# Kernel optimization log

Hardware: AMD Instinct MI355X
Metric: run time of the kernel (lower is better)

## Reference

```python
import jax, jax.numpy as jnp
import numpy as np

H_DIM = 64
GRID = 8
NS = 2.0  # neighborhood_size
S = 256   # number of sequences (scenes)
P = 64    # pedestrians per sequence
EPS = 1e-5


def setup_inputs() -> dict:
    key = jax.random.key(0)
    k = jax.random.split(key, 6)
    N = S * P
    G = GRID * GRID
    h_states = jax.random.normal(k[0], (1, N, H_DIM), jnp.float32)
    end_pos = jax.random.normal(k[1], (N, 2), jnp.float32)
    starts = (jnp.arange(S, dtype=jnp.int32) * P)
    seq_start_end = jnp.stack([starts, starts + P], axis=1)  # (S, 2)
    # mlp_pool: Linear(G*H_DIM -> H_DIM) + BatchNorm1d + ReLU
    W = jax.random.normal(k[2], (G * H_DIM, H_DIM), jnp.float32) / np.sqrt(G * H_DIM)
    b = jnp.zeros((H_DIM,), jnp.float32)
    gamma = jnp.ones((H_DIM,), jnp.float32)
    beta = jnp.zeros((H_DIM,), jnp.float32)
    return {"h_states": h_states, "seq_start_end": seq_start_end, "end_pos": end_pos,
            "W": W, "b": b, "gamma": gamma, "beta": beta}


def reference(h_states, seq_start_end, end_pos, W, b, gamma, beta):
    nseq = seq_start_end.shape[0]          # S (static)
    N = end_pos.shape[0]
    Hd = h_states.shape[-1]
    nped = N // nseq                       # P (static; equal-length sequences)
    G = GRID * GRID
    half = NS / 2.0

    h = h_states.reshape(N, Hd).reshape(nseq, nped, Hd)     # (S, P, H)
    pos = end_pos.reshape(nseq, nped, 2)                    # (S, P, 2)

    # bounds per center pedestrian i
    tl_x = pos[..., 0] - half   # (S, P)
    tl_y = pos[..., 1] + half
    br_x = pos[..., 0] + half
    br_y = pos[..., 1] - half

    # pairwise: axis 1 = center i, axis 2 = other k
    ox = pos[:, None, :, 0]     # (S, 1, P)
    oy = pos[:, None, :, 1]
    cell_x = jnp.floor((ox - tl_x[:, :, None]) / NS * GRID)
    cell_y = jnp.floor((tl_y[:, :, None] - oy) / NS * GRID)
    grid = cell_x + cell_y * GRID                            # (S, P, P)

    oob = ((ox >= br_x[:, :, None]) | (ox <= tl_x[:, :, None]) |
           (oy >= tl_y[:, :, None]) | (oy <= br_y[:, :, None]))
    diag = jnp.eye(nped, dtype=bool)[None]                   # self excluded (within_bound[0::P+1]=1)
    valid = (~oob) & (~diag)

    grid_i = jnp.clip(grid.astype(jnp.int32), 0, G - 1)      # masked entries don't matter
    seq_off = (jnp.arange(nseq, dtype=jnp.int32)[:, None, None] * nped
               + jnp.arange(nped, dtype=jnp.int32)[None, :, None]) * G
    dummy = nseq * nped * G
    ids = jnp.where(valid, seq_off + grid_i, dummy)          # (S, P, P)

    # data for (s, i, k) is hidden of other k (curr_hidden.repeat(num_ped, 1))
    data = jnp.broadcast_to(h[:, None, :, :], (nseq, nped, nped, Hd)).reshape(-1, Hd)
    pooled = jax.ops.segment_sum(data, ids.reshape(-1), num_segments=dummy + 1)[:-1]
    x = pooled.reshape(N, G * Hd)                            # (N, G*H), row i = concat over grid cells

    # mlp_pool: Linear -> BatchNorm1d (train mode, biased var) -> ReLU
    x = x @ W + b
    mu = jnp.mean(x, axis=0)
    var = jnp.mean((x - mu) ** 2, axis=0)
    x = gamma * (x - mu) / jnp.sqrt(var + EPS) + beta
    return jnp.maximum(x, 0.0)
```

## Files before the change

### kernel.cpp

```cpp
#include <hip/hip_runtime.h>
#include <hip/hip_bf16.h>


#define NSEQ 256
#define NTOT (NSEQ*64)
#define EPSV 1e-5f

typedef __attribute__((ext_vector_type(8))) short short8;
typedef __attribute__((ext_vector_type(4))) float f32x4;
typedef unsigned short ushort_t;

__device__ __forceinline__ ushort_t f2b(float f) {
    __hip_bfloat16 h = __float2bfloat16(f);
    return *reinterpret_cast<ushort_t*>(&h);
}
__device__ __forceinline__ unsigned pk2(float a, float b) {
    __hip_bfloat162 t = __float22bfloat162_rn(float2{a, b});
    return *reinterpret_cast<unsigned*>(&t);
}
__device__ __forceinline__ int kperm(int k) {
    return ((k >> 5)*2 + ((k & 7) >> 2))*16 + ((k >> 3) & 3)*4 + (k & 3);
}

__global__ __launch_bounds__(256) void sp_transpose(
    const float* __restrict__ W, short* __restrict__ Wt)
{
    __shared__ __align__(16) float Tl[64*68];
    const int b = blockIdx.x, tid = threadIdx.x;
    const float* wg = W + (size_t)b*4096;
    for (int m = 0; m < 4; ++m) {
        int c = m*256 + tid;
        int k = c >> 4, t0 = (c & 15)*4;
        *(f32x4*)(Tl + k*68 + t0) = *(const f32x4*)(wg + k*64 + t0);
    }
    __syncthreads();
    for (int m = 0; m < 2; ++m) {
        int q = m*256 + tid;
        int col = q >> 3, k0 = (q & 7)*8;
        short8 o;
        #pragma unroll
        for (int i2 = 0; i2 < 8; ++i2)
            o[i2] = (short)f2b(Tl[kperm(k0 + i2)*68 + col]);
        *(short8*)(Wt + ((size_t)(b*64 + col)*64 + k0)) = o;
    }
}

#define SM_CM   9216
#define SM_POS  13312
#define SM_XS1  17408
#define SM_RED  34816
#define SM_TOT  36864

__global__ __launch_bounds__(512, 2) void sp_main(
    const float* __restrict__ h, const float* __restrict__ pos,
    const short* __restrict__ Wt, const float* __restrict__ bvec,
    float* __restrict__ X, float* __restrict__ partials)
{
    __shared__ __align__(16) char smem[SM_TOT];
    ushort_t*      Ht = (ushort_t*)(smem);
    unsigned char* cm = (unsigned char*)(smem + SM_CM);
    float*         px = (float*)(smem + SM_POS);
    float*         py = px + 64;

    const int b    = blockIdx.x;
    const int base = b * 64;
    const int tid  = threadIdx.x;
    const int lane = tid & 63, w = tid >> 6;
    const int ln15 = lane & 15, ln4 = lane >> 4;
    const int xph  = (b >> 3) & 7;

    if (tid < 64) { px[tid] = pos[(base + tid)*2]; py[tid] = pos[(base + tid)*2 + 1]; }
    for (int m = 0; m < 2; ++m) {
        int c = m*512 + tid;
        int j = c >> 4, t0 = (c & 15)*4;
        f32x4 v = *(const f32x4*)(h + (size_t)(base + j)*64 + t0);
        #pragma unroll
        for (int u = 0; u < 4; ++u) Ht[(t0 + u)*72 + j] = f2b(v[u]);
    }
    __syncthreads();

    for (int m = 0; m < 8; ++m) {
        int p = m*512 + tid;
        int i = p >> 6, j = p & 63;
        unsigned char val = 255;
        if (i != j) {
            float ax = px[i], ay = py[i], ox = px[j], oy = py[j];
            float tlx = ax - 1.0f, tly = ay + 1.0f, brx = ax + 1.0f, bry = ay - 1.0f;
            bool oob = (ox >= brx) | (ox <= tlx) | (oy >= tly) | (oy <= bry);
            if (!oob) {
                int g = (int)(floorf((ox - tlx)*4.0f) + floorf((tly - oy)*4.0f)*8.0f);
                g = g < 0 ? 0 : (g > 63 ? 63 : g);
                val = (unsigned char)g;
            }
        }
        cm[i*64 + j] = val;
    }
    __syncthreads();

    short8 hf2[4][2];
    #pragma unroll
    for (int mt = 0; mt < 4; ++mt)
        #pragma unroll
        for (int kt2 = 0; kt2 < 2; ++kt2)
            hf2[mt][kt2] = *(const short8*)(Ht + (mt*16 + ln15)*72 + kt2*32 + ln4*8);
    unsigned cmv[4][2][2];
    #pragma unroll
    for (int rt = 0; rt < 4; ++rt)
        #pragma unroll
        for (int kt = 0; kt < 2; ++kt) {
            const unsigned* cp = (const unsigned*)(cm + (rt*16 + ln15)*64 + kt*32 + ln4*8);
            cmv[rt][kt][0] = cp[0]; cmv[rt][kt][1] = cp[1];
        }

    f32x4 acc[4][4];
    #pragma unroll
    for (int rt = 0; rt < 4; ++rt)
        #pragma unroll
        for (int nt = 0; nt < 4; ++nt) acc[rt][nt] = (f32x4){0.f,0.f,0.f,0.f};

    auto load_cell = [&](short8 (&bw)[2][4], int cidx) {
        const int g = w*8 + ((cidx + xph) & 7);
        const short* wg = Wt + (size_t)g*4096;
        #pragma unroll
        for (int kt = 0; kt < 2; ++kt)
            #pragma unroll
            for (int nt = 0; nt < 4; ++nt)
                bw[kt][nt] = *(const short8*)(wg + (nt*16 + ln15)*64 + kt*32 + ln4*8);
    };
    auto compute_cell = [&](const short8 (&bw)[2][4], int cidx) {
        const int g = w*8 + ((cidx + xph) & 7);
        #pragma unroll
        for (int rt = 0; rt < 4; ++rt) {
            short8 sf[2];
            #pragma unroll
            for (int kt = 0; kt < 2; ++kt)
                #pragma unroll
                for (int u = 0; u < 8; ++u) {
                    unsigned byte = ((u < 4 ? cmv[rt][kt][0] >> (8*u)
                                           : cmv[rt][kt][1] >> (8*(u-4))) & 255u);
                    sf[kt][u] = (byte == (unsigned)g) ? (short)0x3F80 : (short)0;
                }
            f32x4 pt[4];
            #pragma unroll
            for (int mt = 0; mt < 4; ++mt) pt[mt] = (f32x4){0.f,0.f,0.f,0.f};
            #pragma unroll
            for (int kt2 = 0; kt2 < 2; ++kt2)
                #pragma unroll
                for (int mt = 0; mt < 4; ++mt)
                    pt[mt] = __builtin_amdgcn_mfma_f32_16x16x32_bf16(hf2[mt][kt2], sf[kt2], pt[mt], 0, 0, 0);
            #pragma unroll
            for (int kt = 0; kt < 2; ++kt) {
                union { short8 s; unsigned u4[4]; } af;
                af.u4[0] = pk2(pt[2*kt    ][0], pt[2*kt    ][1]);
                af.u4[1] = pk2(pt[2*kt    ][2], pt[2*kt    ][3]);
                af.u4[2] = pk2(pt[2*kt + 1][0], pt[2*kt + 1][1]);
                af.u4[3] = pk2(pt[2*kt + 1][2], pt[2*kt + 1][3]);
                #pragma unroll
                for (int nt = 0; nt < 4; ++nt)
                    acc[rt][nt] = __builtin_amdgcn_mfma_f32_16x16x32_bf16(af.s, bw[kt][nt], acc[rt][nt], 0, 0, 0);
            }
        }
    };

    short8 bwA[2][4], bwB[2][4];
    load_cell(bwA, 0);
    #pragma unroll
    for (int cc = 0; cc < 8; cc += 2) {
        if (cc + 1 < 8) load_cell(bwB, cc + 1);
        compute_cell(bwA, cc);
        if (cc + 2 < 8) load_cell(bwA, cc + 2);
        if (cc + 1 < 8) compute_cell(bwB, cc + 1);
    }
    __syncthreads();

    float* Xs0 = (float*)smem;
    float* Xs1 = (float*)(smem + SM_XS1);
    for (int step = 0; step < 4; ++step) {
        if ((w & 3) == step) {
            float* Xs = (w < 4) ? Xs0 : Xs1;
            #pragma unroll
            for (int rt = 0; rt < 4; ++rt)
                #pragma unroll
                for (int nt = 0; nt < 4; ++nt)
                    #pragma unroll
                    for (int r = 0; r < 4; ++r) {
                        int row = rt*16 + ln4*4 + r;
                        int col = nt*16 + ln15;
                        if (step == 0) Xs[row*68 + col]  = acc[rt][nt][r];
                        else           Xs[row*68 + col] += acc[rt][nt][r];
                    }
        }
        __syncthreads();
    }

    {
        const int row = tid >> 3, c0 = (tid & 7)*8;
        float* xg = X + (size_t)(base + row)*64 + c0;
        #pragma unroll
        for (int q = 0; q < 2; ++q) {
            f32x4 v;
            #pragma unroll
            for (int u = 0; u < 4; ++u) {
                int o = row*68 + c0 + q*4 + u;
                v[u] = Xs0[o] + Xs1[o] + bvec[c0 + q*4 + u];
            }
            *(f32x4*)(xg + q*4) = v;
        }
    }

    {
        float* red1 = (float*)(smem + SM_RED);
        float* red2 = red1 + 256;
        if (tid < 256) {
            int col = tid & 63, rg = tid >> 6;
            float bc = bvec[col], s1 = 0.f, s2 = 0.f;
            for (int ii = 0; ii < 16; ++ii) {
                int o = (rg*16 + ii)*68 + col;
                float xv = Xs0[o] + Xs1[o] + bc;
                s1 += xv; s2 += xv*xv;
            }
            red1[rg*64 + col] = s1;
            red2[rg*64 + col] = s2;
        }
        __syncthreads();
        if (tid < 128) {
            int hs = tid >> 6, c2 = tid & 63;
            const float* r0 = hs ? red2 : red1;
            float v = r0[c2] + r0[64 + c2] + r0[128 + c2] + r0[192 + c2];
            partials[(size_t)b*128 + hs*64 + c2] = v;
        }
    }
}

__global__ __launch_bounds__(256) void sp_finish(
    float* __restrict__ X, const float* __restrict__ partials,
    const float* __restrict__ gamma, const float* __restrict__ beta)
{
    __shared__ float sp0[128], sp1[128];
    __shared__ float scale[64], shift[64];
    const int b = blockIdx.x, tid = threadIdx.x;

    {
        const int slot = tid & 127, hb = tid >> 7;
        float v = 0.f;
        const float* p = partials + (size_t)hb*128*128 + slot;
        #pragma unroll 4
        for (int bb = 0; bb < 128; ++bb) v += p[(size_t)bb*128];
        (hb ? sp1 : sp0)[slot] = v;
    }
    __syncthreads();
    if (tid < 64) {
        const float inv_n = 1.0f / (float)NTOT;
        float s1 = sp0[tid] + sp1[tid];
        float s2 = sp0[64 + tid] + sp1[64 + tid];
        float mu  = s1 * inv_n;
        float var = s2 * inv_n - mu*mu;
        float sc  = gamma[tid] / sqrtf(var + EPSV);
        scale[tid] = sc;
        shift[tid] = beta[tid] - mu*sc;
    }
    __syncthreads();
    #pragma unroll
    for (int q = 0; q < 4; ++q) {
        size_t idx4 = (size_t)b*1024 + q*256 + tid;
        f32x4 v = ((f32x4*)X)[idx4];
        int c0 = ((int)idx4*4) & 63;
        #pragma unroll
        for (int u = 0; u < 4; ++u)
            v[u] = fmaxf(v[u]*scale[c0 + u] + shift[c0 + u], 0.0f);
        ((f32x4*)X)[idx4] = v;
    }
}

extern "C" void kernel_launch(void* const* d_in, const int* in_sizes, int n_in,
                              void* d_out, int out_size, void* d_ws, size_t ws_size,
                              hipStream_t stream)
{
    const float* h     = (const float*)d_in[0];
    const float* pos   = (const float*)d_in[2];
    const float* W     = (const float*)d_in[3];
    const float* bvec  = (const float*)d_in[4];
    const float* gamma = (const float*)d_in[5];
    const float* beta  = (const float*)d_in[6];

    float* X        = (float*)d_out;
    short* Wt       = (short*)d_ws;
    float* partials = (float*)((char*)d_ws + 524288);

    sp_transpose<<<64,   256, 0, stream>>>(W, Wt);
    sp_main     <<<NSEQ, 512, 0, stream>>>(h, pos, Wt, bvec, X, partials);
    sp_finish   <<<NSEQ, 256, 0, stream>>>(X, partials, gamma, beta);
}
```

Measured before the change: 106.2 us.

## Split grid cells across two blocks per sequence and add combine kernel

Each sequence is now handled by two 256-thread blocks, each covering half of the 64 grid cells, which doubles the block count from 256 to 512 and gives the GPU more work to spread across its compute units. The partial 64x64 outputs go to a workspace buffer, and a new combine kernel sums them, adds the bias and computes the per-sequence batch-norm partial sums. The h loads are also kept in registers so they overlap with the cell-map computation before being written to LDS. In exchange, each sequence's cell map is computed twice, there is an extra kernel launch, and the partial outputs make an extra round trip through global memory.

```diff
diff --git a/kernel.cpp b/kernel.cpp
--- a/kernel.cpp
+++ b/kernel.cpp
@@ -48,13 +48,11 @@
 #define SM_CM   9216
 #define SM_POS  13312
 #define SM_XS1  17408
-#define SM_RED  34816
-#define SM_TOT  36864
-
-__global__ __launch_bounds__(512, 2) void sp_main(
+#define SM_TOT  34816
+
+__global__ __launch_bounds__(256, 2) void sp_main(
     const float* __restrict__ h, const float* __restrict__ pos,
-    const short* __restrict__ Wt, const float* __restrict__ bvec,
-    float* __restrict__ X, float* __restrict__ partials)
+    const short* __restrict__ Wt, float* __restrict__ Xpart)
 {
     __shared__ __align__(16) char smem[SM_TOT];
     ushort_t*      Ht = (ushort_t*)(smem);
@@ -62,25 +60,27 @@
     float*         px = (float*)(smem + SM_POS);
     float*         py = px + 64;
 
-    const int b    = blockIdx.x;
-    const int base = b * 64;
-    const int tid  = threadIdx.x;
-    const int lane = tid & 63, w = tid >> 6;
-    const int ln15 = lane & 15, ln4 = lane >> 4;
-    const int xph  = (b >> 3) & 7;
+    const int b     = blockIdx.x;
+    const int s     = b >> 1;
+    const int chalf = b & 1;
+    const int base  = s * 64;
+    const int tid   = threadIdx.x;
+    const int lane  = tid & 63, w = tid >> 6;
+    const int ln15  = lane & 15, ln4 = lane >> 4;
+    const int xph   = (b >> 3) & 7;
 
     if (tid < 64) { px[tid] = pos[(base + tid)*2]; py[tid] = pos[(base + tid)*2 + 1]; }
-    for (int m = 0; m < 2; ++m) {
-        int c = m*512 + tid;
+    f32x4 hreg[4];
+    #pragma unroll
+    for (int m = 0; m < 4; ++m) {
+        int c = m*256 + tid;
         int j = c >> 4, t0 = (c & 15)*4;
-        f32x4 v = *(const f32x4*)(h + (size_t)(base + j)*64 + t0);
-        #pragma unroll
-        for (int u = 0; u < 4; ++u) Ht[(t0 + u)*72 + j] = f2b(v[u]);
-    }
-    __syncthreads();
-
-    for (int m = 0; m < 8; ++m) {
-        int p = m*512 + tid;
+        hreg[m] = *(const f32x4*)(h + (size_t)(base + j)*64 + t0);
+    }
+    __syncthreads();
+
+    for (int m = 0; m < 16; ++m) {
+        int p = m*256 + tid;
         int i = p >> 6, j = p & 63;
         unsigned char val = 255;
         if (i != j) {
@@ -95,6 +95,13 @@
         }
         cm[i*64 + j] = val;
     }
+    #pragma unroll
+    for (int m = 0; m < 4; ++m) {
+        int c = m*256 + tid;
+        int j = c >> 4, t0 = (c & 15)*4;
+        #pragma unroll
+        for (int u = 0; u < 4; ++u) Ht[(t0 + u)*72 + j] = f2b(hreg[m][u]);
+    }
     __syncthreads();
 
     short8 hf2[4][2];
@@ -119,7 +126,7 @@
         for (int nt = 0; nt < 4; ++nt) acc[rt][nt] = (f32x4){0.f,0.f,0.f,0.f};
 
     auto load_cell = [&](short8 (&bw)[2][4], int cidx) {
-        const int g = w*8 + ((cidx + xph) & 7);
+        const int g = chalf*32 + w*8 + ((cidx + xph) & 7);
         const short* wg = Wt + (size_t)g*4096;
         #pragma unroll
         for (int kt = 0; kt < 2; ++kt)
@@ -128,7 +135,7 @@
                 bw[kt][nt] = *(const short8*)(wg + (nt*16 + ln15)*64 + kt*32 + ln4*8);
     };
     auto compute_cell = [&](const short8 (&bw)[2][4], int cidx) {
-        const int g = w*8 + ((cidx + xph) & 7);
+        const int g = chalf*32 + w*8 + ((cidx + xph) & 7);
         #pragma unroll
         for (int rt = 0; rt < 4; ++rt) {
             short8 sf[2];
@@ -175,9 +182,9 @@
 
     float* Xs0 = (float*)smem;
     float* Xs1 = (float*)(smem + SM_XS1);
-    for (int step = 0; step < 4; ++step) {
-        if ((w & 3) == step) {
-            float* Xs = (w < 4) ? Xs0 : Xs1;
+    for (int step = 0; step < 2; ++step) {
+        if ((w & 1) == step) {
+            float* Xs = (w < 2) ? Xs0 : Xs1;
             #pragma unroll
             for (int rt = 0; rt < 4; ++rt)
                 #pragma unroll
@@ -194,41 +201,61 @@
     }
 
     {
-        const int row = tid >> 3, c0 = (tid & 7)*8;
-        float* xg = X + (size_t)(base + row)*64 + c0;
-        #pragma unroll
-        for (int q = 0; q < 2; ++q) {
+        float* xp = Xpart + (size_t)b*4096;
+        const int row = tid >> 2, c0 = (tid & 3)*16;
+        #pragma unroll
+        for (int q = 0; q < 4; ++q) {
             f32x4 v;
             #pragma unroll
             for (int u = 0; u < 4; ++u) {
                 int o = row*68 + c0 + q*4 + u;
-                v[u] = Xs0[o] + Xs1[o] + bvec[c0 + q*4 + u];
+                v[u] = Xs0[o] + Xs1[o];
             }
-            *(f32x4*)(xg + q*4) = v;
-        }
-    }
-
-    {
-        float* red1 = (float*)(smem + SM_RED);
-        float* red2 = red1 + 256;
-        if (tid < 256) {
-            int col = tid & 63, rg = tid >> 6;
-            float bc = bvec[col], s1 = 0.f, s2 = 0.f;
-            for (int ii = 0; ii < 16; ++ii) {
-                int o = (rg*16 + ii)*68 + col;
-                float xv = Xs0[o] + Xs1[o] + bc;
-                s1 += xv; s2 += xv*xv;
-            }
-            red1[rg*64 + col] = s1;
-            red2[rg*64 + col] = s2;
-        }
-        __syncthreads();
-        if (tid < 128) {
-            int hs = tid >> 6, c2 = tid & 63;
-            const float* r0 = hs ? red2 : red1;
-            float v = r0[c2] + r0[64 + c2] + r0[128 + c2] + r0[192 + c2];
-            partials[(size_t)b*128 + hs*64 + c2] = v;
-        }
+            *(f32x4*)(xp + row*64 + c0 + q*4) = v;
+        }
+    }
+}
+
+__global__ __launch_bounds__(256) void sp_combine(
+    const float* __restrict__ Xpart, const float* __restrict__ bvec,
+    float* __restrict__ X, float* __restrict__ partials)
+{
+    __shared__ float red1[16*64], red2[16*64];
+    const int s = blockIdx.x, tid = threadIdx.x;
+    const f32x4* Xa = (const f32x4*)(Xpart + (size_t)(2*s    )*4096);
+    const f32x4* Xb = (const f32x4*)(Xpart + (size_t)(2*s + 1)*4096);
+    f32x4* Xo = (f32x4*)(X + (size_t)s*4096);
+
+    const int c0 = (tid & 15)*4;
+    float s1[4] = {0.f,0.f,0.f,0.f}, s2[4] = {0.f,0.f,0.f,0.f};
+    float bb[4];
+    #pragma unroll
+    for (int u = 0; u < 4; ++u) bb[u] = bvec[c0 + u];
+    #pragma unroll
+    for (int q = 0; q < 4; ++q) {
+        int idx4 = q*256 + tid;
+        f32x4 va = Xa[idx4], vb = Xb[idx4], v;
+        #pragma unroll
+        for (int u = 0; u < 4; ++u) {
+            v[u] = va[u] + vb[u] + bb[u];
+            s1[u] += v[u]; s2[u] += v[u]*v[u];
+        }
+        Xo[idx4] = v;
+    }
+    const int grp = tid >> 4;
+    #pragma unroll
+    for (int u = 0; u < 4; ++u) {
+        red1[grp*64 + c0 + u] = s1[u];
+        red2[grp*64 + c0 + u] = s2[u];
+    }
+    __syncthreads();
+    if (tid < 128) {
+        int hs = tid >> 6, c = tid & 63;
+        const float* r0 = hs ? red2 : red1;
+        float v = 0.f;
+        #pragma unroll
+        for (int g2 = 0; g2 < 16; ++g2) v += r0[g2*64 + c];
+        partials[(size_t)s*128 + hs*64 + c] = v;
     }
 }
 
@@ -285,9 +312,11 @@
 
     float* X        = (float*)d_out;
     short* Wt       = (short*)d_ws;
-    float* partials = (float*)((char*)d_ws + 524288);
-
-    sp_transpose<<<64,   256, 0, stream>>>(W, Wt);
-    sp_main     <<<NSEQ, 512, 0, stream>>>(h, pos, Wt, bvec, X, partials);
+    float* Xpart    = (float*)((char*)d_ws + 524288);
+    float* partials = (float*)((char*)d_ws + 524288 + 8388608);
+
+    sp_transpose<<<64,  256, 0, stream>>>(W, Wt);
+    sp_main     <<<512, 256, 0, stream>>>(h, pos, Wt, Xpart);
+    sp_combine  <<<NSEQ, 256, 0, stream>>>(Xpart, bvec, X, partials);
     sp_finish   <<<NSEQ, 256, 0, stream>>>(X, partials, gamma, beta);
 }
```

Result: slower. 112.6 us (+6.0%).
